# Optimization experiments

Measured on AMD Instinct MI355X. Metric: run time of the kernel, lower is better.

## Reference

```python
import jax, jax.numpy as jnp
import numpy as np

STEPS = 2
P_TOPP = 0.9
TAU = 1.0
LN_EPS = 1e-5


def _top_p_attention(pooled, W1, W2, W3):
    # pooled: (N, C). Bilinear scores -> softmax -> nucleus (top-p) sparsify -> renorm.
    e1 = pooled @ W1.T                      # (N, d)
    e3 = pooled @ W3.T                      # (N, d)
    logits = (e1 @ W2.T) @ e3.T / TAU       # (N, N)
    attn = jax.nn.softmax(logits, axis=-1)
    srt = jnp.sort(attn, axis=-1)[:, ::-1]  # descending
    csum = jnp.cumsum(srt, axis=-1)
    keep = (csum - srt) < P_TOPP            # keep entries whose exclusive cum-prob < p
    thr = jnp.min(jnp.where(keep, srt, jnp.inf), axis=-1, keepdims=True)
    masked = jnp.where(attn >= thr, attn, 0.0)
    return masked / jnp.clip(jnp.sum(masked, axis=-1, keepdims=True), 1e-12)


def _layernorm(h, gamma, beta):
    mu = jnp.mean(h, axis=-1, keepdims=True)
    var = jnp.mean(jnp.square(h - mu), axis=-1, keepdims=True)
    return (h - mu) * jax.lax.rsqrt(var + LN_EPS) * gamma + beta


def _forward(x, prior, W1, W2, W3, prior_fwd_w, adaptive_w, ln_gamma, ln_beta, alpha):
    # Row-normalised prior (forward diffusion operator)
    Rf = prior / jnp.clip(jnp.sum(prior, axis=1, keepdims=True), 1e-12)
    Xf = x
    Xa = x
    residual = jnp.zeros_like(x)
    for idx in range(STEPS):
        pooled = jnp.mean(Xa, axis=1)                      # protein axis pooling -> (N_P, C)
        attn = _top_p_attention(pooled, W1, W2, W3)        # (N_P, N_P)
        Xf = jnp.einsum('ij,jkc->ikc', Rf, Xf)
        Xa = jnp.einsum('ij,jkc->ikc', attn, Xa)
        delta = jnp.einsum('ikc,dc->ikd', Xf, prior_fwd_w[idx]) \
              + jnp.einsum('ikc,dc->ikd', Xa, adaptive_w[idx])
        residual = residual + delta                        # dropout is identity in eval mode
    gate = jax.nn.sigmoid(alpha)                           # (1,)
    return _layernorm(x + gate * residual, ln_gamma, ln_beta)


def setup_inputs() -> dict:
    key = jax.random.key(0)
    ks = jax.random.split(key, 8)
    N_P, N_C, C, D = 2048, 64, 128, 64
    x = jax.random.normal(ks[0], (N_P, N_C, C), dtype=jnp.float32)
    prior = jax.random.uniform(ks[1], (N_P, N_P), dtype=jnp.float32)
    W1 = jax.random.normal(ks[2], (D, C), dtype=jnp.float32) / np.sqrt(C)
    W2 = jax.random.normal(ks[3], (D, D), dtype=jnp.float32) / np.sqrt(D)
    W3 = jax.random.normal(ks[4], (D, C), dtype=jnp.float32) / np.sqrt(C)
    prior_fwd_w = jax.random.normal(ks[5], (STEPS, C, C), dtype=jnp.float32) / np.sqrt(C)
    adaptive_w = jax.random.normal(ks[6], (STEPS, C, C), dtype=jnp.float32) / np.sqrt(C)
    ln_gamma = jnp.ones((C,), dtype=jnp.float32)
    ln_beta = jnp.zeros((C,), dtype=jnp.float32)
    alpha = jnp.zeros((1,), dtype=jnp.float32)
    return {"x": x, "prior": prior, "W1": W1, "W2": W2, "W3": W3,
            "prior_fwd_w": prior_fwd_w, "adaptive_w": adaptive_w,
            "ln_gamma": ln_gamma, "ln_beta": ln_beta, "alpha": alpha}


def reference(x, prior, W1, W2, W3, prior_fwd_w, adaptive_w, ln_gamma, ln_beta, alpha):
    return _forward(x, prior, W1, W2, W3, prior_fwd_w, adaptive_w, ln_gamma, ln_beta, alpha)
```

## Files before the change

kernel.cpp:

```cpp
#include <hip/hip_runtime.h>

typedef unsigned short u16;
typedef __attribute__((ext_vector_type(8))) short short8;
typedef __attribute__((ext_vector_type(4))) float f32x4;
typedef __attribute__((ext_vector_type(16))) float f32x16;

#define AS1 __attribute__((address_space(1)))
#define AS3 __attribute__((address_space(3)))

__device__ __forceinline__ void async_cp16(const void* g, void* l) {
  __builtin_amdgcn_global_load_lds((const AS1 unsigned int*)g, (AS3 unsigned int*)l, 16, 0, 0);
}

__device__ __forceinline__ u16 f2bf(float f) {
  union { float f; unsigned u; } v; v.f = f;
  unsigned r = v.u + 0x7fffu + ((v.u >> 16) & 1u);
  return (u16)(r >> 16);
}
__device__ __forceinline__ float bf2f(u16 h) {
  union { unsigned u; float f; } v; v.u = ((unsigned)h) << 16;
  return v.f;
}

template<int MODE>
__global__ __launch_bounds__(256, 2) void gemm32(
    const u16* __restrict__ A, const u16* __restrict__ B,
    int M, int N, int K,
    u16* __restrict__ Crow, int crow_ld, int crow_coloff,
    u16* __restrict__ Ct, int ct_ld)
{
  __shared__ u16 smem[12288];
  u16* sA = smem;
  u16* sB = smem + 4096;
  const int tid  = threadIdx.x;
  const int lane = tid & 63;
  const int wid  = tid >> 6;
  const int m0 = blockIdx.y * 128;
  const int n0 = blockIdx.x * 256;
  const int wm = (wid >> 1) * 64;
  const int wn = (wid & 1) * 128;
  const int l31  = lane & 31;
  const int half = lane >> 5;
  const int pl   = (l31 & 3) ^ ((l31 >> 2) & 3);

  f32x16 acc[2][4];
#pragma unroll
  for (int i = 0; i < 2; i++)
#pragma unroll
    for (int j = 0; j < 4; j++)
#pragma unroll
      for (int r = 0; r < 16; r++) acc[i][j][r] = 0.f;

  const int r4 = tid >> 2;
  const int cc = tid & 3;
  const int g8 = (cc ^ ((r4 & 3) ^ ((r4 >> 2) & 3))) * 8;
  const u16* gA0 = A + (size_t)(m0 + r4) * K + g8;
  const u16* gA1 = A + (size_t)(m0 + 64 + r4) * K + g8;
  const u16* gB0 = B + (size_t)(n0 + r4) * K + g8;
  const u16* gB1 = B + (size_t)(n0 + 64 + r4) * K + g8;
  const u16* gB2 = B + (size_t)(n0 + 128 + r4) * K + g8;
  const u16* gB3 = B + (size_t)(n0 + 192 + r4) * K + g8;
  u16* lA0 = sA + wid * 512;
  u16* lA1 = sA + 2048 + wid * 512;
  u16* lB0 = sB + wid * 512;
  u16* lB1 = sB + 2048 + wid * 512;
  u16* lB2 = sB + 4096 + wid * 512;
  u16* lB3 = sB + 6144 + wid * 512;

  for (int k0 = 0; k0 < K; k0 += 32) {
    async_cp16(gA0 + k0, lA0);
    async_cp16(gA1 + k0, lA1);
    async_cp16(gB0 + k0, lB0);
    async_cp16(gB1 + k0, lB1);
    async_cp16(gB2 + k0, lB2);
    async_cp16(gB3 + k0, lB3);
    __syncthreads();
#pragma unroll
    for (int s = 0; s < 2; s++) {
      const int kc = ((s * 2 + half) ^ pl) * 8;
      short8 aF[2], bF[4];
#pragma unroll
      for (int i = 0; i < 2; i++)
        aF[i] = *(const short8*)(sA + (wm + i * 32 + l31) * 32 + kc);
#pragma unroll
      for (int j = 0; j < 4; j++)
        bF[j] = *(const short8*)(sB + (wn + j * 32 + l31) * 32 + kc);
#pragma unroll
      for (int i = 0; i < 2; i++)
#pragma unroll
        for (int j = 0; j < 4; j++)
          acc[i][j] = __builtin_amdgcn_mfma_f32_32x32x16_bf16(aF[i], bF[j], acc[i][j], 0, 0, 0);
    }
    __syncthreads();
  }

  u16* T = smem;

#pragma unroll
  for (int pr = 0; pr < 2; pr++)
#pragma unroll
    for (int pc = 0; pc < 2; pc++) {
      if (((wid >> 1) == pr) && ((wid & 1) == pc)) {
#pragma unroll
        for (int i = 0; i < 2; i++)
#pragma unroll
          for (int j = 0; j < 4; j++)
#pragma unroll
            for (int r = 0; r < 16; r++) {
              const int rrow = i * 32 + (r & 3) + 8 * (r >> 2) + 4 * half;
              T[rrow * 136 + j * 32 + l31] = f2bf(acc[i][j][r]);
            }
      }
      __syncthreads();
      {
        const int row = tid >> 2, q = tid & 3;
        const size_t crow = (size_t)(m0 + pr * 64 + row) * (N >> 7) + (n0 >> 7) + pc;
        u16* dst = Crow + crow * (size_t)crow_ld + crow_coloff + q * 32;
        const u16* src = T + row * 136 + q * 32;
#pragma unroll
        for (int u = 0; u < 4; u++) ((float4*)dst)[u] = ((const float4*)src)[u];
      }
      __syncthreads();
    }

  if constexpr (MODE == 1) {
#pragma unroll
    for (int p = 0; p < 4; p++) {
      if ((wid & 1) == (p >> 1)) {
        const int jb = (p & 1) * 2;
#pragma unroll
        for (int i = 0; i < 2; i++)
#pragma unroll
          for (int jj = 0; jj < 2; jj++)
#pragma unroll
            for (int r = 0; r < 16; r++) {
              const int nloc = jj * 32 + l31;
              const int mcol = wm + i * 32 + (r & 3) + 8 * (r >> 2) + 4 * half;
              T[nloc * 136 + mcol] = f2bf(acc[i][jb + jj][r]);
            }
      }
      __syncthreads();
      {
        const int row = tid >> 2, q = tid & 3;
        u16* dst = Ct + (size_t)(n0 + p * 64 + row) * ct_ld + m0 + q * 32;
        const u16* src = T + row * 136 + q * 32;
#pragma unroll
        for (int u = 0; u < 4; u++) ((float4*)dst)[u] = ((const float4*)src)[u];
      }
      __syncthreads();
    }
  }
}

template<int MODE>
__global__ __launch_bounds__(256) void gemm_bt(
    const u16* __restrict__ A, const u16* __restrict__ B,
    int M, int N, int K,
    float* __restrict__ Cf,
    u16* __restrict__ Crow, int crow_ld, int crow_coloff)
{
  extern __shared__ char smemc[];
  u16* sA = (u16*)smemc;
  u16* sB = (u16*)(smemc + 8192);
  const int tid  = threadIdx.x;
  const int lane = tid & 63;
  const int wid  = tid >> 6;
  const int m0 = blockIdx.y * 128;
  const int n0 = blockIdx.x * 128;
  const int wm = (wid >> 1) * 64;
  const int wn = (wid & 1) * 64;
  const int ml = lane & 15;
  const int qd = lane >> 4;

  f32x4 acc[4][4];
  const f32x4 zero = {0.f, 0.f, 0.f, 0.f};
#pragma unroll
  for (int i = 0; i < 4; i++)
#pragma unroll
    for (int j = 0; j < 4; j++) acc[i][j] = zero;

  const int r4 = tid >> 2;
  const int c4 = (tid & 3) * 8;
  const u16* gA0 = A + (size_t)(m0 + r4) * K + c4;
  const u16* gA1 = A + (size_t)(m0 + 64 + r4) * K + c4;
  const u16* gB0 = B + (size_t)(n0 + r4) * K + c4;
  const u16* gB1 = B + (size_t)(n0 + 64 + r4) * K + c4;
  u16* lA0 = sA + wid * 512;
  u16* lA1 = sA + 2048 + wid * 512;
  u16* lB0 = sB + wid * 512;
  u16* lB1 = sB + 2048 + wid * 512;

  for (int k0 = 0; k0 < K; k0 += 32) {
    async_cp16(gA0 + k0, lA0);
    async_cp16(gA1 + k0, lA1);
    async_cp16(gB0 + k0, lB0);
    async_cp16(gB1 + k0, lB1);
    __syncthreads();
    short8 af[4], bfr[4];
#pragma unroll
    for (int i = 0; i < 4; i++)
      af[i] = *(const short8*)(sA + (wm + i * 16 + ml) * 32 + qd * 8);
#pragma unroll
    for (int j = 0; j < 4; j++)
      bfr[j] = *(const short8*)(sB + (wn + j * 16 + ml) * 32 + qd * 8);
#pragma unroll
    for (int i = 0; i < 4; i++)
#pragma unroll
      for (int j = 0; j < 4; j++)
        acc[i][j] = __builtin_amdgcn_mfma_f32_16x16x32_bf16(af[i], bfr[j], acc[i][j], 0, 0, 0);
    __syncthreads();
  }

  if constexpr (MODE == 3) {
#pragma unroll
    for (int i = 0; i < 4; i++) {
      const int mr = m0 + wm + i * 16 + qd * 4;
#pragma unroll
      for (int j = 0; j < 4; j++) {
        const int nc = n0 + wn + j * 16 + ml;
        float* p = Cf + (size_t)mr * N + nc;
#pragma unroll
        for (int r = 0; r < 4; r++) p[(size_t)r * N] = acc[i][j][r];
      }
    }
  } else {
    u16* T = (u16*)smemc;
#pragma unroll
    for (int i = 0; i < 4; i++)
#pragma unroll
      for (int j = 0; j < 4; j++)
#pragma unroll
        for (int r = 0; r < 4; r++)
          T[(wm + i * 16 + qd * 4 + r) * 136 + wn + j * 16 + ml] = f2bf(acc[i][j][r]);
    __syncthreads();
    const int row = tid >> 1, halfr = tid & 1;
    const size_t crow = (size_t)(m0 + row) * (N >> 7) + (n0 >> 7);
    u16* dst = Crow + crow * (size_t)crow_ld + crow_coloff + halfr * 64;
    const u16* src = T + row * 136 + halfr * 64;
#pragma unroll
    for (int u = 0; u < 8; u++) ((float4*)dst)[u] = ((const float4*)src)[u];
  }
}

__global__ void rowsum_k(const float* __restrict__ prior, float* __restrict__ rs) {
  const int i = blockIdx.x, t = threadIdx.x;
  const float* p = prior + (size_t)i * 2048;
  float s = 0.f;
  for (int j = t; j < 2048; j += 256) s += p[j];
  __shared__ float red[256];
  red[t] = s; __syncthreads();
  for (int o = 128; o; o >>= 1) { if (t < o) red[t] += red[t + o]; __syncthreads(); }
  if (t == 0) rs[i] = red[0];
}

__global__ void convprior_k(const float4* __restrict__ prior, const float* __restrict__ rs,
                            ushort4* __restrict__ dst) {
  const int idx = blockIdx.x * 256 + threadIdx.x;
  const float inv = 1.0f / rs[idx >> 9];
  const float4 v = prior[idx];
  ushort4 o;
  o.x = f2bf(v.x * inv); o.y = f2bf(v.y * inv); o.z = f2bf(v.z * inv); o.w = f2bf(v.w * inv);
  dst[idx] = o;
}

__global__ void convx_k(const float* __restrict__ x, u16* __restrict__ xt) {
  __shared__ float S[64][65];
  const int t = threadIdx.x;
  const int j0 = blockIdx.y * 64;
  const int n0 = blockIdx.x * 64;
  const int rr = t >> 4, cxc = (t & 15) * 4;
#pragma unroll
  for (int p = 0; p < 4; p++) {
    const float4 v = *(const float4*)(x + (size_t)(j0 + rr + p * 16) * 8192 + n0 + cxc);
    S[rr + p * 16][cxc + 0] = v.x; S[rr + p * 16][cxc + 1] = v.y;
    S[rr + p * 16][cxc + 2] = v.z; S[rr + p * 16][cxc + 3] = v.w;
  }
  __syncthreads();
  const int nl = t >> 2, ch = (t & 3) * 16;
  alignas(16) u16 tmp[16];
#pragma unroll
  for (int u = 0; u < 16; u++) tmp[u] = f2bf(S[ch + u][nl]);
  float4* dst = (float4*)(xt + (size_t)(n0 + nl) * 2048 + j0 + ch);
  dst[0] = ((const float4*)tmp)[0];
  dst[1] = ((const float4*)tmp)[1];
}

__global__ void convw_k(const float* __restrict__ pw, const float* __restrict__ aw,
                        u16* __restrict__ btc) {
  const int idx = blockIdx.x * 256 + threadIdx.x;
  const int k = idx & 255, d = (idx >> 8) & 127, s = idx >> 15;
  const float v = (k < 128) ? aw[(s * 128 + d) * 128 + k] : pw[(s * 128 + d) * 128 + (k - 128)];
  btc[idx] = f2bf(v);
}

__global__ void pooled1_k(const float* __restrict__ x, float* __restrict__ pooled) {
  const int i = blockIdx.x, t = threadIdx.x;
  const int c = t & 127, h = t >> 7;
  const float* base = x + (size_t)i * 8192 + c;
  float s = 0.f;
  for (int k = h * 32; k < h * 32 + 32; k++) s += base[(size_t)k * 128];
  __shared__ float red[256];
  red[t] = s; __syncthreads();
  if (t < 128) pooled[i * 128 + t] = (red[t] + red[t + 128]) * (1.f / 64.f);
}

__global__ void pooled2_k(const u16* __restrict__ comb, float* __restrict__ pooled) {
  const int i = blockIdx.x, t = threadIdx.x;
  const int c = t & 127, h = t >> 7;
  const u16* base = comb + (size_t)i * 64 * 256 + c;
  float s = 0.f;
  for (int k = h * 32; k < h * 32 + 32; k++) s += bf2f(base[(size_t)k * 256]);
  __shared__ float red[256];
  red[t] = s; __syncthreads();
  if (t < 128) pooled[i * 128 + t] = (red[t] + red[t + 128]) * (1.f / 64.f);
}

__global__ void epre_k(const float* __restrict__ pooled,
                       const float* __restrict__ W1, const float* __restrict__ W2,
                       const float* __restrict__ W3,
                       u16* __restrict__ e3b, u16* __restrict__ fb) {
  const int i = blockIdx.x, d = threadIdx.x;
  __shared__ float pr[128], e1s[64];
  pr[d] = pooled[i * 128 + d];
  pr[d + 64] = pooled[i * 128 + 64 + d];
  __syncthreads();
  float s1 = 0.f, s3 = 0.f;
  for (int c = 0; c < 128; c++) {
    const float p = pr[c];
    s1 += p * W1[d * 128 + c];
    s3 += p * W3[d * 128 + c];
  }
  e1s[d] = s1;
  e3b[i * 64 + d] = f2bf(s3);
  __syncthreads();
  float sf = 0.f;
  for (int dd = 0; dd < 64; dd++) sf += e1s[dd] * W2[d * 64 + dd];
  fb[i * 64 + d] = f2bf(sf);
}

__device__ __forceinline__ float waveRedSum(float v) {
#pragma unroll
  for (int o = 1; o < 64; o <<= 1) v += __shfl_xor(v, o);
  return __shfl(v, 0);
}
__device__ __forceinline__ float waveRedMax(float v) {
#pragma unroll
  for (int o = 1; o < 64; o <<= 1) v = fmaxf(v, __shfl_xor(v, o));
  return __shfl(v, 0);
}

__global__ __launch_bounds__(256) void topp_k(const float* __restrict__ logits,
                                              u16* __restrict__ attnb) {
  const int w = threadIdx.x >> 6, l = threadIdx.x & 63;
  const int i = blockIdx.x * 4 + w;
  const float4* row = (const float4*)(logits + (size_t)i * 2048);
  float E[32];
  float mx = -1e30f;
#pragma unroll
  for (int k = 0; k < 8; k++) {
    const float4 v = row[k * 64 + l];
    E[k * 4 + 0] = v.x; E[k * 4 + 1] = v.y; E[k * 4 + 2] = v.z; E[k * 4 + 3] = v.w;
    mx = fmaxf(fmaxf(mx, fmaxf(v.x, v.y)), fmaxf(v.z, v.w));
  }
  mx = waveRedMax(mx);
  float S = 0.f;
#pragma unroll
  for (int u = 0; u < 32; u++) { E[u] = __expf(E[u] - mx); S += E[u]; }
  S = waveRedSum(S);
  const float target = 0.9f * S;
  float lo = 0.f, hi = 1.f;
  for (int it = 0; it < 32; ++it) {
    const float mid = 0.5f * (lo + hi);
    float g = 0.f;
#pragma unroll
    for (int u = 0; u < 32; u++) g += (E[u] > mid) ? E[u] : 0.f;
    g = waveRedSum(g);
    const bool below = (g < target);
    hi = below ? mid : hi;
    lo = below ? lo : mid;
  }
  float Sk = 0.f;
#pragma unroll
  for (int u = 0; u < 32; u++) Sk += (E[u] > lo) ? E[u] : 0.f;
  Sk = waveRedSum(Sk);
  const float inv = 1.f / Sk;
  u16* dst = attnb + (size_t)i * 2048;
#pragma unroll
  for (int k = 0; k < 8; k++) {
    ushort4 o;
    o.x = f2bf(E[k * 4 + 0] > lo ? E[k * 4 + 0] * inv : 0.f);
    o.y = f2bf(E[k * 4 + 1] > lo ? E[k * 4 + 1] * inv : 0.f);
    o.z = f2bf(E[k * 4 + 2] > lo ? E[k * 4 + 2] * inv : 0.f);
    o.w = f2bf(E[k * 4 + 3] > lo ? E[k * 4 + 3] * inv : 0.f);
    *(ushort4*)(dst + k * 256 + l * 4) = o;
  }
}

__global__ void ln_k(const float* __restrict__ x,
                     const u16* __restrict__ d1, const u16* __restrict__ d2,
                     float* __restrict__ out,
                     const float* __restrict__ gamma, const float* __restrict__ beta,
                     const float* __restrict__ alpha) {
  const int wid = threadIdx.x >> 6, lane = threadIdx.x & 63;
  const float gate = 1.f / (1.f + expf(-alpha[0]));
  const float2 g = ((const float2*)gamma)[lane];
  const float2 b = ((const float2*)beta)[lane];
#pragma unroll
  for (int rr = 0; rr < 2; ++rr) {
    const size_t row = (size_t)blockIdx.x * 8 + wid * 2 + rr;
    const float2 xv = ((const float2*)(x + row * 128))[lane];
    const ushort2 r1 = ((const ushort2*)(d1 + row * 128))[lane];
    const ushort2 r2 = ((const ushort2*)(d2 + row * 128))[lane];
    const float h0 = xv.x + gate * (bf2f(r1.x) + bf2f(r2.x));
    const float h1 = xv.y + gate * (bf2f(r1.y) + bf2f(r2.y));
    float s = h0 + h1;
#pragma unroll
    for (int o = 32; o; o >>= 1) s += __shfl_down(s, o);
    const float mu = __shfl(s, 0) * (1.f / 128.f);
    const float d0 = h0 - mu, dd1 = h1 - mu;
    float vs = d0 * d0 + dd1 * dd1;
#pragma unroll
    for (int o = 32; o; o >>= 1) vs += __shfl_down(vs, o);
    const float rstd = rsqrtf(__shfl(vs, 0) * (1.f / 128.f) + 1e-5f);
    float2* op = (float2*)(out + row * 128);
    float2 ov;
    ov.x = d0 * rstd * g.x + b.x;
    ov.y = dd1 * rstd * g.y + b.y;
    op[lane] = ov;
  }
}

extern "C" void kernel_launch(void* const* d_in, const int* in_sizes, int n_in,
                              void* d_out, int out_size, void* d_ws, size_t ws_size,
                              hipStream_t stream) {
  const float* x     = (const float*)d_in[0];
  const float* prior = (const float*)d_in[1];
  const float* W1    = (const float*)d_in[2];
  const float* W2    = (const float*)d_in[3];
  const float* W3    = (const float*)d_in[4];
  const float* Pw    = (const float*)d_in[5];
  const float* Aw    = (const float*)d_in[6];
  const float* gamma = (const float*)d_in[7];
  const float* beta  = (const float*)d_in[8];
  const float* alpha = (const float*)d_in[9];
  float* out = (float*)d_out;

  char* w = (char*)d_ws;
  u16*   Xt_x   = (u16*)(w);
  u16*   XtA    = (u16*)(w + 33554432);
  u16*   XtF    = (u16*)(w + 67108864);
  u16*   comb   = (u16*)(w + 100663296);
  u16*   priorS = (u16*)(w + 167772160);
  u16*   attnb  = (u16*)(w + 176160768);
  float* pooled = (float*)(w + 184549376);
  u16*   e3b    = (u16*)(w + 185597952);
  u16*   fb     = (u16*)(w + 186122240);
  float* rs     = (float*)(w + 186646528);
  u16*   btc    = (u16*)(w + 186654720);
  float* logits1 = (float*)(w + 33554432);
  float* logits2 = (float*)(w);
  u16*   d1      = (u16*)(w);
  u16*   d2      = (u16*)(w + 33554432);
  (void)in_sizes; (void)n_in; (void)ws_size;

  rowsum_k   <<<2048, 256, 0, stream>>>(prior, rs);
  convprior_k<<<4096, 256, 0, stream>>>((const float4*)prior, rs, (ushort4*)priorS);
  convx_k    <<<dim3(128, 32), 256, 0, stream>>>(x, Xt_x);
  convw_k    <<<256, 256, 0, stream>>>(Pw, Aw, btc);

  pooled1_k  <<<2048, 256, 0, stream>>>(x, pooled);
  epre_k     <<<2048, 64, 0, stream>>>(pooled, W1, W2, W3, e3b, fb);
  gemm_bt<3> <<<dim3(16, 16), 256, 16384, stream>>>(fb, e3b, 2048, 2048, 64,
                                                    logits1, nullptr, 0, 0);
  topp_k     <<<512, 256, 0, stream>>>(logits1, attnb);

  gemm32<1><<<dim3(32, 16), 256, 0, stream>>>(attnb,  Xt_x, 2048, 8192, 2048,
                                              comb, 256, 0,   XtA, 2048);
  gemm32<1><<<dim3(32, 16), 256, 0, stream>>>(priorS, Xt_x, 2048, 8192, 2048,
                                              comb, 256, 128, XtF, 2048);

  pooled2_k  <<<2048, 256, 0, stream>>>(comb, pooled);
  epre_k     <<<2048, 64, 0, stream>>>(pooled, W1, W2, W3, e3b, fb);
  gemm_bt<3> <<<dim3(16, 16), 256, 16384, stream>>>(fb, e3b, 2048, 2048, 64,
                                                    logits2, nullptr, 0, 0);
  topp_k     <<<512, 256, 0, stream>>>(logits2, attnb);

  gemm_bt<2><<<dim3(1, 1024), 256, 34816, stream>>>(comb, btc, 131072, 128, 256,
                                                    nullptr, d1, 128, 0);

  gemm32<2><<<dim3(32, 16), 256, 0, stream>>>(attnb,  XtA, 2048, 8192, 2048,
                                              comb, 256, 0,   nullptr, 0);
  gemm32<2><<<dim3(32, 16), 256, 0, stream>>>(priorS, XtF, 2048, 8192, 2048,
                                              comb, 256, 128, nullptr, 0);

  gemm_bt<2><<<dim3(1, 1024), 256, 34816, stream>>>(comb, btc + 32768, 131072, 128, 256,
                                                    nullptr, d2, 128, 0);

  ln_k<<<16384, 256, 0, stream>>>(x, d1, d2, out, gamma, beta, alpha);
}
```

Measured before the change: 696.2 us.

## Enlarge diffusion GEMM tile to 256x256 with 128x128 per-wave accumulators

The big 2048x8192x2048 propagation GEMMs move from 128x256 block tiles to 256x256 tiles. Each wave now holds a 4x4 grid of 32x32 MFMA accumulators, and the epilogue staging buffer is widened to match. This raises arithmetic intensity per LDS load and halves the number of blocks, which cuts global and LDS traffic per FLOP. In exchange, occupancy drops to one block per CU because of 256 accumulator registers, and the grid shrinks to 256 blocks, roughly one wave of work on 256 CUs. The single-stage load/sync loop gets no latency hiding from a second resident block.

```diff
diff --git a/kernel.cpp b/kernel.cpp
--- a/kernel.cpp
+++ b/kernel.cpp
@@ -23,29 +23,29 @@
 }
 
 template<int MODE>
-__global__ __launch_bounds__(256, 2) void gemm32(
+__global__ __launch_bounds__(256, 1) void gemm32(
     const u16* __restrict__ A, const u16* __restrict__ B,
     int M, int N, int K,
     u16* __restrict__ Crow, int crow_ld, int crow_coloff,
     u16* __restrict__ Ct, int ct_ld)
 {
-  __shared__ u16 smem[12288];
+  __shared__ u16 smem[17408];
   u16* sA = smem;
-  u16* sB = smem + 4096;
+  u16* sB = smem + 8192;
   const int tid  = threadIdx.x;
   const int lane = tid & 63;
   const int wid  = tid >> 6;
-  const int m0 = blockIdx.y * 128;
+  const int m0 = blockIdx.y * 256;
   const int n0 = blockIdx.x * 256;
-  const int wm = (wid >> 1) * 64;
+  const int wm = (wid >> 1) * 128;
   const int wn = (wid & 1) * 128;
   const int l31  = lane & 31;
   const int half = lane >> 5;
   const int pl   = (l31 & 3) ^ ((l31 >> 2) & 3);
 
-  f32x16 acc[2][4];
-#pragma unroll
-  for (int i = 0; i < 2; i++)
+  f32x16 acc[4][4];
+#pragma unroll
+  for (int i = 0; i < 4; i++)
 #pragma unroll
     for (int j = 0; j < 4; j++)
 #pragma unroll
@@ -54,39 +54,34 @@
   const int r4 = tid >> 2;
   const int cc = tid & 3;
   const int g8 = (cc ^ ((r4 & 3) ^ ((r4 >> 2) & 3))) * 8;
-  const u16* gA0 = A + (size_t)(m0 + r4) * K + g8;
-  const u16* gA1 = A + (size_t)(m0 + 64 + r4) * K + g8;
-  const u16* gB0 = B + (size_t)(n0 + r4) * K + g8;
-  const u16* gB1 = B + (size_t)(n0 + 64 + r4) * K + g8;
-  const u16* gB2 = B + (size_t)(n0 + 128 + r4) * K + g8;
-  const u16* gB3 = B + (size_t)(n0 + 192 + r4) * K + g8;
-  u16* lA0 = sA + wid * 512;
-  u16* lA1 = sA + 2048 + wid * 512;
-  u16* lB0 = sB + wid * 512;
-  u16* lB1 = sB + 2048 + wid * 512;
-  u16* lB2 = sB + 4096 + wid * 512;
-  u16* lB3 = sB + 6144 + wid * 512;
+  const u16* gA[4]; const u16* gB[4];
+  u16* lA[4]; u16* lB[4];
+#pragma unroll
+  for (int q = 0; q < 4; q++) {
+    gA[q] = A + (size_t)(m0 + q * 64 + r4) * K + g8;
+    gB[q] = B + (size_t)(n0 + q * 64 + r4) * K + g8;
+    lA[q] = sA + q * 2048 + wid * 512;
+    lB[q] = sB + q * 2048 + wid * 512;
+  }
 
   for (int k0 = 0; k0 < K; k0 += 32) {
-    async_cp16(gA0 + k0, lA0);
-    async_cp16(gA1 + k0, lA1);
-    async_cp16(gB0 + k0, lB0);
-    async_cp16(gB1 + k0, lB1);
-    async_cp16(gB2 + k0, lB2);
-    async_cp16(gB3 + k0, lB3);
+#pragma unroll
+    for (int q = 0; q < 4; q++) async_cp16(gA[q] + k0, lA[q]);
+#pragma unroll
+    for (int q = 0; q < 4; q++) async_cp16(gB[q] + k0, lB[q]);
     __syncthreads();
 #pragma unroll
     for (int s = 0; s < 2; s++) {
       const int kc = ((s * 2 + half) ^ pl) * 8;
-      short8 aF[2], bF[4];
-#pragma unroll
-      for (int i = 0; i < 2; i++)
+      short8 aF[4], bF[4];
+#pragma unroll
+      for (int i = 0; i < 4; i++)
         aF[i] = *(const short8*)(sA + (wm + i * 32 + l31) * 32 + kc);
 #pragma unroll
       for (int j = 0; j < 4; j++)
         bF[j] = *(const short8*)(sB + (wn + j * 32 + l31) * 32 + kc);
 #pragma unroll
-      for (int i = 0; i < 2; i++)
+      for (int i = 0; i < 4; i++)
 #pragma unroll
         for (int j = 0; j < 4; j++)
           acc[i][j] = __builtin_amdgcn_mfma_f32_32x32x16_bf16(aF[i], bF[j], acc[i][j], 0, 0, 0);
@@ -97,55 +92,54 @@
   u16* T = smem;
 
 #pragma unroll
-  for (int pr = 0; pr < 2; pr++)
-#pragma unroll
-    for (int pc = 0; pc < 2; pc++) {
-      if (((wid >> 1) == pr) && ((wid & 1) == pc)) {
-#pragma unroll
-        for (int i = 0; i < 2; i++)
-#pragma unroll
-          for (int j = 0; j < 4; j++)
+  for (int p = 0; p < 4; p++) {
+    if ((wid >> 1) == (p >> 1)) {
+      const int ib = (p & 1) * 2;
+#pragma unroll
+      for (int ii = 0; ii < 2; ii++)
+#pragma unroll
+        for (int j = 0; j < 4; j++)
+#pragma unroll
+          for (int r = 0; r < 16; r++) {
+            const int rrow = ii * 32 + (r & 3) + 8 * (r >> 2) + 4 * half;
+            T[rrow * 272 + wn + j * 32 + l31] = f2bf(acc[ib + ii][j][r]);
+          }
+    }
+    __syncthreads();
+    {
+      const int row = tid >> 2, q = tid & 3;
+      const size_t crow = (size_t)(m0 + p * 64 + row) * (N >> 7) + (n0 >> 7) + (q >> 1);
+      u16* dst = Crow + crow * (size_t)crow_ld + crow_coloff + (q & 1) * 64;
+      const u16* src = T + row * 272 + q * 64;
+#pragma unroll
+      for (int u = 0; u < 8; u++) ((float4*)dst)[u] = ((const float4*)src)[u];
+    }
+    __syncthreads();
+  }
+
+  if constexpr (MODE == 1) {
+#pragma unroll
+    for (int p = 0; p < 4; p++) {
+      if ((wid & 1) == (p >> 1)) {
+        const int jb = (p & 1) * 2;
+#pragma unroll
+        for (int jj = 0; jj < 2; jj++)
+#pragma unroll
+          for (int i = 0; i < 4; i++)
 #pragma unroll
             for (int r = 0; r < 16; r++) {
-              const int rrow = i * 32 + (r & 3) + 8 * (r >> 2) + 4 * half;
-              T[rrow * 136 + j * 32 + l31] = f2bf(acc[i][j][r]);
+              const int nloc = jj * 32 + l31;
+              const int mcol = wm + i * 32 + (r & 3) + 8 * (r >> 2) + 4 * half;
+              T[nloc * 272 + mcol] = f2bf(acc[i][jb + jj][r]);
             }
       }
       __syncthreads();
       {
         const int row = tid >> 2, q = tid & 3;
-        const size_t crow = (size_t)(m0 + pr * 64 + row) * (N >> 7) + (n0 >> 7) + pc;
-        u16* dst = Crow + crow * (size_t)crow_ld + crow_coloff + q * 32;
-        const u16* src = T + row * 136 + q * 32;
-#pragma unroll
-        for (int u = 0; u < 4; u++) ((float4*)dst)[u] = ((const float4*)src)[u];
-      }
-      __syncthreads();
-    }
-
-  if constexpr (MODE == 1) {
-#pragma unroll
-    for (int p = 0; p < 4; p++) {
-      if ((wid & 1) == (p >> 1)) {
-        const int jb = (p & 1) * 2;
-#pragma unroll
-        for (int i = 0; i < 2; i++)
-#pragma unroll
-          for (int jj = 0; jj < 2; jj++)
-#pragma unroll
-            for (int r = 0; r < 16; r++) {
-              const int nloc = jj * 32 + l31;
-              const int mcol = wm + i * 32 + (r & 3) + 8 * (r >> 2) + 4 * half;
-              T[nloc * 136 + mcol] = f2bf(acc[i][jb + jj][r]);
-            }
-      }
-      __syncthreads();
-      {
-        const int row = tid >> 2, q = tid & 3;
-        u16* dst = Ct + (size_t)(n0 + p * 64 + row) * ct_ld + m0 + q * 32;
-        const u16* src = T + row * 136 + q * 32;
-#pragma unroll
-        for (int u = 0; u < 4; u++) ((float4*)dst)[u] = ((const float4*)src)[u];
+        u16* dst = Ct + (size_t)(n0 + p * 64 + row) * ct_ld + m0 + q * 64;
+        const u16* src = T + row * 272 + q * 64;
+#pragma unroll
+        for (int u = 0; u < 8; u++) ((float4*)dst)[u] = ((const float4*)src)[u];
       }
       __syncthreads();
     }
@@ -474,10 +468,10 @@
                                                     logits1, nullptr, 0, 0);
   topp_k     <<<512, 256, 0, stream>>>(logits1, attnb);
 
-  gemm32<1><<<dim3(32, 16), 256, 0, stream>>>(attnb,  Xt_x, 2048, 8192, 2048,
-                                              comb, 256, 0,   XtA, 2048);
-  gemm32<1><<<dim3(32, 16), 256, 0, stream>>>(priorS, Xt_x, 2048, 8192, 2048,
-                                              comb, 256, 128, XtF, 2048);
+  gemm32<1><<<dim3(32, 8), 256, 0, stream>>>(attnb,  Xt_x, 2048, 8192, 2048,
+                                             comb, 256, 0,   XtA, 2048);
+  gemm32<1><<<dim3(32, 8), 256, 0, stream>>>(priorS, Xt_x, 2048, 8192, 2048,
+                                             comb, 256, 128, XtF, 2048);
 
   pooled2_k  <<<2048, 256, 0, stream>>>(comb, pooled);
   epre_k     <<<2048, 64, 0, stream>>>(pooled, W1, W2, W3, e3b, fb);
@@ -488,10 +482,10 @@
   gemm_bt<2><<<dim3(1, 1024), 256, 34816, stream>>>(comb, btc, 131072, 128, 256,
                                                     nullptr, d1, 128, 0);
 
-  gemm32<2><<<dim3(32, 16), 256, 0, stream>>>(attnb,  XtA, 2048, 8192, 2048,
-                                              comb, 256, 0,   nullptr, 0);
-  gemm32<2><<<dim3(32, 16), 256, 0, stream>>>(priorS, XtF, 2048, 8192, 2048,
-                                              comb, 256, 128, nullptr, 0);
+  gemm32<2><<<dim3(32, 8), 256, 0, stream>>>(attnb,  XtA, 2048, 8192, 2048,
+                                             comb, 256, 0,   nullptr, 0);
+  gemm32<2><<<dim3(32, 8), 256, 0, stream>>>(priorS, XtF, 2048, 8192, 2048,
+                                             comb, 256, 128, nullptr, 0);
 
   gemm_bt<2><<<dim3(1, 1024), 256, 34816, stream>>>(comb, btc + 32768, 131072, 128, 256,
                                                     nullptr, d2, 128, 0);
```

New measurement: 935.9 us. +34.4%, slower.
